# Kernel optimization log

Hardware: AMD Instinct MI355X
Metric: run time of the kernel (lower is better)

The kernel has to match this reference:

```python
import jax, jax.numpy as jnp
import numpy as np


def _conv2d_valid(x, w):
    # x: (N, C, H, W), w: (O, C, kH, kW) -> (N, O, H-kH+1, W-kW+1)
    return jax.lax.conv_general_dilated(
        x, w, window_strides=(1, 1), padding='VALID',
        dimension_numbers=('NCHW', 'OIHW', 'NCHW'))


def setup_inputs() -> dict:
    key = jax.random.key(0)
    kx, ky = jax.random.split(key)
    x = jax.random.normal(kx, (16, 64, 128, 128), dtype=jnp.float32)
    y = jax.random.normal(ky, (64, 64, 16, 16), dtype=jnp.float32)
    return {"x": x, "y": y}


def reference(x, y):
    # Normalize each of the K kernels to unit L2 norm (sum over C, kH, kW).
    normed_y = y / jnp.sqrt(jnp.sum(y * y, axis=(1, 2, 3), keepdims=True))
    # Per-window L2 norm of x via ones-kernel box conv over x^2.
    ones_kernel = jnp.ones(y.shape, dtype=x.dtype)
    x_norm = jnp.sqrt(_conv2d_valid(x * x, ones_kernel))
    # Normalized cross-correlation, clamped at zero.
    diss = _conv2d_valid(x, normed_y) / x_norm
    return jax.nn.relu(diss)
```

## Files before the change

### kernel.cpp

```cpp
#include <hip/hip_runtime.h>
#include <stdint.h>

#define GAS __attribute__((address_space(1)))
#define LAS __attribute__((address_space(3)))

typedef __attribute__((ext_vector_type(8))) short short8;
typedef __attribute__((ext_vector_type(4))) float float4v;
typedef __attribute__((ext_vector_type(4))) unsigned int uint4v;

__device__ __forceinline__ unsigned short f2bf(float f) {
  union { float f; unsigned int u; } v; v.f = f;
  unsigned int r = v.u + 0x7fffu + ((v.u >> 16) & 1u);
  return (unsigned short)(r >> 16);
}

__device__ __forceinline__ void async_g2l16(const void* g, void* l) {
  __builtin_amdgcn_global_load_lds((const GAS unsigned int*)g,
                                   (LAS unsigned int*)l, 16, 0, 0);
}

__device__ __forceinline__ void vmem_drain() {
  asm volatile("s_waitcnt vmcnt(0)" ::: "memory");
}

__global__ void kprep(const float* __restrict__ x, const float* __restrict__ y,
                      unsigned short* __restrict__ x_t, unsigned short* __restrict__ y_t2,
                      float* __restrict__ s) {
  int b = blockIdx.x;
  int tid = threadIdx.x;
  if (b >= 2048) {
    int o = b - 2048;
    const float* yo = y + o * 16384;
    float sm = 0.f;
    for (int idx = tid; idx < 16384; idx += 256) { float v = yo[idx]; sm += v * v; }
    for (int off = 32; off; off >>= 1) sm += __shfl_down(sm, off, 64);
    __shared__ float red[4];
    if ((tid & 63) == 0) red[tid >> 6] = sm;
    __syncthreads();
    float rn = 1.0f / sqrtf(red[0] + red[1] + red[2] + red[3]);
    int og = o >> 4, ol = o & 15;
    for (int idx = tid; idx < 16384; idx += 256) {
      int c = idx >> 8, dy = (idx >> 4) & 15, dx = idx & 15;
      int t = dy * 16 + dx;
      int cb = c >> 5, q = (c >> 3) & 3, j = c & 7;
      size_t dst = (size_t)t * 4096 + (size_t)(og * 2 + cb) * 512 + (q * 16 + ol) * 8 + j;
      y_t2[dst] = f2bf(yo[idx] * rn);
    }
    return;
  }
  int h = b & 127, n = b >> 7;
  __shared__ __align__(16) unsigned short tb[8192];
  __shared__ float sb[256];
  const float* xb = x + ((size_t)n * 64) * 16384 + h * 128;
  int w = tid & 127, half = tid >> 7;
  float acc = 0.f;
#pragma unroll
  for (int cs = 0; cs < 4; ++cs) {
    short8 tmp;
#pragma unroll
    for (int j = 0; j < 8; ++j) {
      int c = half * 32 + cs * 8 + j;
      float v = xb[(size_t)c * 16384 + w];
      tmp[j] = (short)f2bf(v);
      acc += v * v;
    }
    int chunk = (half * 4 + cs) ^ (w & 7);
    *(short8*)(tb + w * 64 + chunk * 8) = tmp;
  }
  sb[tid] = acc;
  __syncthreads();
  uint4v* dst = (uint4v*)(x_t + ((size_t)(n * 128 + h)) * 8192);
  const uint4v* src = (const uint4v*)tb;
  for (int idx = tid; idx < 1024; idx += 256) dst[idx] = src[idx];
  if (tid < 128) s[((size_t)(n * 128 + h)) * 128 + tid] = sb[tid] + sb[tid + 128];
}

__global__ void knorm_x(const float* __restrict__ s, float* __restrict__ invn) {
  int i = blockIdx.x, n = blockIdx.y;
  int tid = threadIdx.x;
  __shared__ float colsum[128];
  const float* sp = s + ((size_t)(n * 128 + i)) * 128;
  float a = 0.f;
#pragma unroll
  for (int dy = 0; dy < 16; ++dy) a += sp[dy * 128 + tid];
  colsum[tid] = a;
  __syncthreads();
  if (tid < 113) {
    float acc = 0.f;
#pragma unroll
    for (int dx = 0; dx < 16; ++dx) acc += colsum[tid + dx];
    invn[((size_t)n * 113 + i) * 113 + tid] = 1.0f / sqrtf(acc);
  }
}

__launch_bounds__(256, 4)
__global__ void kconv(const unsigned short* __restrict__ x_t,
                      const unsigned short* __restrict__ y_t2,
                      const float* __restrict__ invn,
                      float* __restrict__ out) {
  int lin = blockIdx.y * 113 + blockIdx.x;
  int wg = (lin & 7) * 226 + (lin >> 3);
  int i = wg % 113;
  int n = wg / 113;
  int tid = threadIdx.x;
  int lane = tid & 63, wave = tid >> 6;
  int lane15 = lane & 15, q = lane >> 4;
  int wrow = wave >> 1, wcol = wave & 1;

  __shared__ __align__(16) char smem[32768];
  char* const A0 = smem;
  char* const A1 = smem + 16384;

  const char* xrow0 = (const char*)(x_t + ((size_t)(n * 128 + i)) * 8192);

  auto stageA = [&](int dy, char* buf) {
    const char* src = xrow0 + (size_t)dy * 16384;
#pragma unroll
    for (int it = 0; it < 4; ++it) {
      int chunk = it * 256 + wave * 64;
      async_g2l16(src + (chunk + lane) * 16, buf + chunk * 16);
    }
  };

  const short8* ybase = (const short8*)(y_t2 + (size_t)wcol * 2048 + (size_t)lane * 8);
  auto loadB = [&](int t, short8 bf[2][2]) {
    const short8* p = ybase + (size_t)t * 512;
    bf[0][0] = p[0];
    bf[0][1] = p[64];
    bf[1][0] = p[128];
    bf[1][1] = p[192];
  };

  float4v acc[4][2];
#pragma unroll
  for (int mt = 0; mt < 4; ++mt)
#pragma unroll
    for (int nt = 0; nt < 2; ++nt) acc[mt][nt] = (float4v){0.f, 0.f, 0.f, 0.f};

  int abase[4];
#pragma unroll
  for (int mt = 0; mt < 4; ++mt) abase[mt] = (wrow * 64 + mt * 16 + lane15) * 128;

  short8 b0[2][2], b1[2][2];
  stageA(0, A0);
  loadB(0, b0);
  vmem_drain();
  __syncthreads();

#pragma unroll 1
  for (int dy = 0; dy < 16; ++dy) {
    char* Ab = (dy & 1) ? A1 : A0;
    if (dy < 15) {
      __builtin_amdgcn_sched_barrier(0);
      stageA(dy + 1, (dy & 1) ? A0 : A1);
      __builtin_amdgcn_sched_barrier(0);
    }
#pragma unroll
    for (int dx = 0; dx < 16; ++dx) {
      int t = dy * 16 + dx;
      short8(&bc)[2][2] = (dx & 1) ? b1 : b0;
      short8(&bn)[2][2] = (dx & 1) ? b0 : b1;
      if (t < 255) loadB(t + 1, bn);
      int xr = (lane15 + dx) & 7;
      __builtin_amdgcn_s_setprio(1);
#pragma unroll
      for (int cb = 0; cb < 2; ++cb) {
        int aoff = dx * 128 + (((q + cb * 4) ^ xr) << 4);
#pragma unroll
        for (int mt = 0; mt < 4; ++mt) {
          short8 a = *(const short8*)(Ab + abase[mt] + aoff);
          acc[mt][0] = __builtin_amdgcn_mfma_f32_16x16x32_bf16(a, bc[0][cb], acc[mt][0], 0, 0, 0);
          acc[mt][1] = __builtin_amdgcn_mfma_f32_16x16x32_bf16(a, bc[1][cb], acc[mt][1], 0, 0, 0);
        }
      }
      __builtin_amdgcn_s_setprio(0);
    }
    asm volatile("s_waitcnt vmcnt(4)" ::: "memory");
    __syncthreads();
  }

  float* cs = (float*)smem;
  float* ivs = cs + 4352;
  const float* ivp = invn + ((size_t)n * 113 + i) * 113;
  if (tid < 128) ivs[tid] = (tid < 113) ? ivp[tid] : 0.f;
  float* op = out + (size_t)n * 64 * 12769 + (size_t)i * 113;
#pragma unroll 1
  for (int p = 0; p < 2; ++p) {
    if (wcol == p) {
#pragma unroll
      for (int mt = 0; mt < 4; ++mt)
#pragma unroll
        for (int nt = 0; nt < 2; ++nt) {
          int row = nt * 16 + lane15;
          int j0 = wrow * 64 + mt * 16 + q * 4;
          *(float4v*)(cs + row * 132 + j0) = acc[mt][nt];
        }
    }
    __syncthreads();
    for (int idx = tid; idx < 4096; idx += 256) {
      int o2 = idx >> 7, j = idx & 127;
      if (j < 113) {
        float v = cs[o2 * 132 + j] * ivs[j];
        op[(size_t)(p * 32 + o2) * 12769 + j] = fmaxf(v, 0.f);
      }
    }
    __syncthreads();
  }
}

extern "C" void kernel_launch(void* const* d_in, const int* in_sizes, int n_in,
                              void* d_out, int out_size, void* d_ws, size_t ws_size,
                              hipStream_t stream) {
  const float* x = (const float*)d_in[0];
  const float* y = (const float*)d_in[1];
  float* out = (float*)d_out;
  char* ws = (char*)d_ws;
  unsigned short* x_t = (unsigned short*)ws;
  unsigned short* y_t2 = (unsigned short*)(ws + 33554432);
  float* s = (float*)(ws + 35651584);
  float* invn = (float*)(ws + 36700160);

  hipLaunchKernelGGL(kprep, dim3(2112), dim3(256), 0, stream, x, y, x_t, y_t2, s);
  hipLaunchKernelGGL(knorm_x, dim3(113, 16), dim3(128), 0, stream, s, invn);
  hipLaunchKernelGGL(kconv, dim3(113, 16), dim3(256), 0, stream, x_t, y_t2, invn, out);
}
```

Measured before the change: 546.0 us.

## Fuse window-norm kernel into conv and store epilogue directly from registers

```diff
diff --git a/kernel.cpp b/kernel.cpp
--- a/kernel.cpp
+++ b/kernel.cpp
@@ -75,28 +75,10 @@
   if (tid < 128) s[((size_t)(n * 128 + h)) * 128 + tid] = sb[tid] + sb[tid + 128];
 }
 
-__global__ void knorm_x(const float* __restrict__ s, float* __restrict__ invn) {
-  int i = blockIdx.x, n = blockIdx.y;
-  int tid = threadIdx.x;
-  __shared__ float colsum[128];
-  const float* sp = s + ((size_t)(n * 128 + i)) * 128;
-  float a = 0.f;
-#pragma unroll
-  for (int dy = 0; dy < 16; ++dy) a += sp[dy * 128 + tid];
-  colsum[tid] = a;
-  __syncthreads();
-  if (tid < 113) {
-    float acc = 0.f;
-#pragma unroll
-    for (int dx = 0; dx < 16; ++dx) acc += colsum[tid + dx];
-    invn[((size_t)n * 113 + i) * 113 + tid] = 1.0f / sqrtf(acc);
-  }
-}
-
 __launch_bounds__(256, 4)
 __global__ void kconv(const unsigned short* __restrict__ x_t,
                       const unsigned short* __restrict__ y_t2,
-                      const float* __restrict__ invn,
+                      const float* __restrict__ s,
                       float* __restrict__ out) {
   int lin = blockIdx.y * 113 + blockIdx.x;
   int wg = (lin & 7) * 226 + (lin >> 3);
@@ -108,6 +90,8 @@
   int wrow = wave >> 1, wcol = wave & 1;
 
   __shared__ __align__(16) char smem[32768];
+  __shared__ float csum[128];
+  __shared__ __align__(16) float ivs[128];
   char* const A0 = smem;
   char* const A1 = smem + 16384;
 
@@ -144,6 +128,24 @@
   short8 b0[2][2], b1[2][2];
   stageA(0, A0);
   loadB(0, b0);
+
+  {
+    const float* sp = s + ((size_t)(n * 128 + i)) * 128;
+    if (tid < 128) {
+      float a = 0.f;
+#pragma unroll
+      for (int dy = 0; dy < 16; ++dy) a += sp[dy * 128 + tid];
+      csum[tid] = a;
+    }
+    __syncthreads();
+    if (tid < 113) {
+      float a = 0.f;
+#pragma unroll
+      for (int dx = 0; dx < 16; ++dx) a += csum[tid + dx];
+      ivs[tid] = 1.0f / sqrtf(a);
+    }
+  }
+
   vmem_drain();
   __syncthreads();
 
@@ -162,7 +164,6 @@
       short8(&bn)[2][2] = (dx & 1) ? b0 : b1;
       if (t < 255) loadB(t + 1, bn);
       int xr = (lane15 + dx) & 7;
-      __builtin_amdgcn_s_setprio(1);
 #pragma unroll
       for (int cb = 0; cb < 2; ++cb) {
         int aoff = dx * 128 + (((q + cb * 4) ^ xr) << 4);
@@ -173,38 +174,38 @@
           acc[mt][1] = __builtin_amdgcn_mfma_f32_16x16x32_bf16(a, bc[1][cb], acc[mt][1], 0, 0, 0);
         }
       }
-      __builtin_amdgcn_s_setprio(0);
     }
     asm volatile("s_waitcnt vmcnt(4)" ::: "memory");
     __syncthreads();
   }
 
-  float* cs = (float*)smem;
-  float* ivs = cs + 4352;
-  const float* ivp = invn + ((size_t)n * 113 + i) * 113;
-  if (tid < 128) ivs[tid] = (tid < 113) ? ivp[tid] : 0.f;
   float* op = out + (size_t)n * 64 * 12769 + (size_t)i * 113;
-#pragma unroll 1
-  for (int p = 0; p < 2; ++p) {
-    if (wcol == p) {
-#pragma unroll
-      for (int mt = 0; mt < 4; ++mt)
-#pragma unroll
-        for (int nt = 0; nt < 2; ++nt) {
-          int row = nt * 16 + lane15;
-          int j0 = wrow * 64 + mt * 16 + q * 4;
-          *(float4v*)(cs + row * 132 + j0) = acc[mt][nt];
-        }
-    }
-    __syncthreads();
-    for (int idx = tid; idx < 4096; idx += 256) {
-      int o2 = idx >> 7, j = idx & 127;
-      if (j < 113) {
-        float v = cs[o2 * 132 + j] * ivs[j];
-        op[(size_t)(p * 32 + o2) * 12769 + j] = fmaxf(v, 0.f);
+  int obase = wcol * 32 + lane15;
+  int jb = wrow * 64 + q * 4;
+#pragma unroll
+  for (int mt = 0; mt < 4; ++mt) {
+    int j0 = jb + mt * 16;
+    if (j0 <= 108) {
+      float4v iv = *(const float4v*)(ivs + j0);
+#pragma unroll
+      for (int nt = 0; nt < 2; ++nt) {
+        int o = obase + nt * 16;
+        float4v v = acc[mt][nt];
+        float4v r;
+        r[0] = fmaxf(v[0] * iv[0], 0.f);
+        r[1] = fmaxf(v[1] * iv[1], 0.f);
+        r[2] = fmaxf(v[2] * iv[2], 0.f);
+        r[3] = fmaxf(v[3] * iv[3], 0.f);
+        *(float4v*)(op + (size_t)o * 12769 + j0) = r;
       }
-    }
-    __syncthreads();
+    } else if (j0 == 112) {
+      float ivv = ivs[112];
+#pragma unroll
+      for (int nt = 0; nt < 2; ++nt) {
+        int o = obase + nt * 16;
+        op[(size_t)o * 12769 + 112] = fmaxf(acc[mt][nt][0] * ivv, 0.f);
+      }
+    }
   }
 }
 
@@ -218,9 +219,7 @@
   unsigned short* x_t = (unsigned short*)ws;
   unsigned short* y_t2 = (unsigned short*)(ws + 33554432);
   float* s = (float*)(ws + 35651584);
-  float* invn = (float*)(ws + 36700160);
 
   hipLaunchKernelGGL(kprep, dim3(2112), dim3(256), 0, stream, x, y, x_t, y_t2, s);
-  hipLaunchKernelGGL(knorm_x, dim3(113, 16), dim3(128), 0, stream, s, invn);
-  hipLaunchKernelGGL(kconv, dim3(113, 16), dim3(256), 0, stream, x_t, y_t2, invn, out);
-}
+  hipLaunchKernelGGL(kconv, dim3(113, 16), dim3(256), 0, stream, x_t, y_t2, s, out);
+}
```

After: 531.7 us. -2.6%, faster.
